# Kernel optimization log

Hardware: AMD Instinct MI355X
Metric: run time of the kernel (lower is better)

The kernel has to match this reference:

```python
import jax, jax.numpy as jnp
import numpy as np

H = 4                 # num_heads
GATE_NORM = 16.0      # gate_logit_normalizer
EPS = 1e-5            # RMSNorm eps


def setup_inputs() -> dict:
    key = jax.random.key(0)
    ks = jax.random.split(key, 12)
    B, T, D = 8, 4096, 1024
    Dk_total, Dv_total, Dlow = D // 2, D, 16

    def w(k, shape, fan_in):
        return jax.random.normal(k, shape, dtype=jnp.float32) * (fan_in ** -0.5)

    return {
        "x": jax.random.normal(ks[0], (B, T, D), dtype=jnp.float32),
        "Wq": w(ks[1], (D, Dk_total), D),
        "Wk": w(ks[2], (D, Dk_total), D),
        "Wv": w(ks[3], (D, Dv_total), D),
        "gk_w1": w(ks[4], (D, Dlow), D),
        "gk_w2": w(ks[5], (Dlow, Dk_total), Dlow),
        "gk_b2": jnp.zeros((Dk_total,), dtype=jnp.float32),
        "Wg": w(ks[6], (D, Dv_total), D),
        "g_norm_w": jnp.ones((Dv_total // H,), dtype=jnp.float32),
        "Wo": w(ks[7], (Dv_total, D), Dv_total),
    }


def _gla_forward(x, Wq, Wk, Wv, gk_w1, gk_w2, gk_b2, Wg, g_norm_w, Wo):
    B, T, D = x.shape
    Dk = Wq.shape[1] // H
    Dv = Wv.shape[1] // H

    q = (x @ Wq).reshape(B, T, H, Dk) * (Dk ** -0.5)
    k = (x @ Wk).reshape(B, T, H, Dk)
    v = (x @ Wv).reshape(B, T, H, Dv)
    # low-rank gate logits -> log-space decay gk (<= 0)
    gk = jax.nn.log_sigmoid((x @ gk_w1) @ gk_w2 + gk_b2) / GATE_NORM
    gk = gk.reshape(B, T, H, Dk)

    # recurrent gated linear attention:
    #   S_t = exp(gk_t)[:, None] * S_{t-1} + k_t^T v_t ;  o_t = q_t @ S_t
    def step(S, qkvg):
        qt, kt, vt, gt = qkvg          # each [B, H, Dk|Dv]
        S = jnp.exp(gt)[..., None] * S + kt[..., None] * vt[..., None, :]
        ot = jnp.einsum("bhk,bhkv->bhv", qt, S)
        return S, ot

    S0 = jnp.zeros((B, H, Dk, Dv), dtype=x.dtype)
    tm = lambda a: jnp.swapaxes(a, 0, 1)  # [B,T,...] -> [T,B,...]
    _, o = jax.lax.scan(step, S0, (tm(q), tm(k), tm(v), tm(gk)))
    o = jnp.swapaxes(o, 0, 1)            # [B, T, H, Dv]

    # output gate: RMSNorm(o) * swish(g), per head
    g = (x @ Wg).reshape(B, T, H, Dv)
    o = o * jax.lax.rsqrt(jnp.mean(o * o, axis=-1, keepdims=True) + EPS) * g_norm_w
    o = o * (g * jax.nn.sigmoid(g))
    return o.reshape(B, T, H * Dv) @ Wo


def reference(x, Wq, Wk, Wv, gk_w1, gk_w2, gk_b2, Wg, g_norm_w, Wo):
    return _gla_forward(x, Wq, Wk, Wv, gk_w1, gk_w2, gk_b2, Wg, g_norm_w, Wo)
```

## Files before the change

kernel.cpp:

```cpp
#include <hip/hip_runtime.h>
#include <hip/hip_bf16.h>
#include <cstdint>
#include <cstddef>

typedef __hip_bfloat16 bf16;
typedef __attribute__((ext_vector_type(8))) short short8;
typedef __attribute__((ext_vector_type(4))) float floatx4;

__device__ __forceinline__ void gload_lds16(const void* g, void* l) {
  __builtin_amdgcn_global_load_lds(
      (__attribute__((address_space(1))) void*)(uintptr_t)g,
      (__attribute__((address_space(3))) void*)l, 16, 0, 0);
}

__device__ __forceinline__ short f2bbits(float f) {
  bf16 h = __float2bfloat16(f);
  return __builtin_bit_cast(short, h);
}
__device__ __forceinline__ float b2f(short s) {
  return __bfloat162float(__builtin_bit_cast(bf16, s));
}

__global__ __launch_bounds__(256) void convert_x(const float* __restrict__ x,
                                                 bf16* __restrict__ xb) {
  size_t i = ((size_t)blockIdx.x * 256 + threadIdx.x) * 8;
  float4 f0 = *(const float4*)(x + i);
  float4 f1 = *(const float4*)(x + i + 4);
  short8 r;
  r[0] = f2bbits(f0.x); r[1] = f2bbits(f0.y); r[2] = f2bbits(f0.z); r[3] = f2bbits(f0.w);
  r[4] = f2bbits(f1.x); r[5] = f2bbits(f1.y); r[6] = f2bbits(f1.z); r[7] = f2bbits(f1.w);
  *(short8*)(xb + i) = r;
}

__global__ __launch_bounds__(256) void transpose_w(const float* __restrict__ src,
                                                   bf16* __restrict__ dst, int cols) {
  __shared__ float tile[32][33];
  int n0 = blockIdx.x * 32, k0 = blockIdx.y * 32;
  int tx = threadIdx.x & 31, ty = threadIdx.x >> 5;
#pragma unroll
  for (int i = 0; i < 32; i += 8) {
    int kk = k0 + ty + i, nn = n0 + tx;
    tile[ty + i][tx] = (nn < cols) ? src[(size_t)kk * cols + nn] : 0.0f;
  }
  __syncthreads();
#pragma unroll
  for (int i = 0; i < 32; i += 8) {
    int nn = n0 + ty + i, kk = k0 + tx;
    if (nn < cols) dst[(size_t)nn * 1024 + kk] = __float2bfloat16(tile[tx][ty + i]);
  }
}

#define BARR __builtin_amdgcn_s_barrier()
#define WAITV(n) asm volatile("s_waitcnt vmcnt(" #n ")" ::: "memory")

#define STA(buf, h, tau) do { \
  gload_lds16(pA + (size_t)(h) * K64 + (size_t)(tau) * 64, \
              &lds[(buf) * 16384 + (h) * 8192 + w * 512]); \
  gload_lds16(pA + K128 + (size_t)(h) * K64 + (size_t)(tau) * 64, \
              &lds[(buf) * 16384 + (h) * 8192 + 4096 + w * 512]); \
} while (0)

#define STB(buf, h, tau) do { \
  gload_lds16(pB + (size_t)(h) * K32 + (size_t)(tau) * 64, \
              &lds[32768 + (buf) * 16384 + (h) * 8192 + w * 512]); \
  gload_lds16(pB + K128 + (size_t)(h) * K32 + (size_t)(tau) * 64, \
              &lds[32768 + (buf) * 16384 + (h) * 8192 + 4096 + w * 512]); \
} while (0)

#define LDA(mh, buf) do { \
  _Pragma("unroll") \
  for (int mp = 0; mp < 4; ++mp) { \
    const short* p_ = &lds[(buf) * 16384 + (mh) * 8192 + aRow + mp * 1024]; \
    a[mp][0] = *(const short8*)(p_ + g0); \
    a[mp][1] = *(const short8*)(p_ + g1); \
  } \
} while (0)

#define LDB(nh, buf, d0, d1) do { \
  const short* p_ = &lds[(buf) * 16384 + (nh) * 8192 + bRow]; \
  d0[0] = *(const short8*)(p_ + g0); \
  d0[1] = *(const short8*)(p_ + g1); \
  d1[0] = *(const short8*)(p_ + 1024 + g0); \
  d1[1] = *(const short8*)(p_ + 1024 + g1); \
} while (0)

#define MQ(MB, NB, d0, d1) do { \
  __builtin_amdgcn_s_setprio(1); \
  _Pragma("unroll") \
  for (int mp = 0; mp < 4; ++mp) { \
    acc[(MB) + mp][(NB)] = __builtin_amdgcn_mfma_f32_16x16x32_bf16(a[mp][0], d0[0], acc[(MB) + mp][(NB)], 0, 0, 0); \
    acc[(MB) + mp][(NB)] = __builtin_amdgcn_mfma_f32_16x16x32_bf16(a[mp][1], d0[1], acc[(MB) + mp][(NB)], 0, 0, 0); \
    acc[(MB) + mp][(NB) + 1] = __builtin_amdgcn_mfma_f32_16x16x32_bf16(a[mp][0], d1[0], acc[(MB) + mp][(NB) + 1], 0, 0, 0); \
    acc[(MB) + mp][(NB) + 1] = __builtin_amdgcn_mfma_f32_16x16x32_bf16(a[mp][1], d1[1], acc[(MB) + mp][(NB) + 1], 0, 0, 0); \
  } \
  __builtin_amdgcn_s_setprio(0); \
} while (0)

__global__ __launch_bounds__(512, 2) void gemm256(
    const bf16* __restrict__ A, const bf16* __restrict__ Bt, const int K,
    const int nTN, const int mode,
    float* __restrict__ oq, float* __restrict__ okk, bf16* __restrict__ ov,
    bf16* __restrict__ ogg, float* __restrict__ oo) {
  extern __shared__ __align__(16) short lds[];
  const int tid = threadIdx.x;
  const int w = tid >> 6, lane = tid & 63;
  const int wr = w >> 2, wc = w & 3;
  const int l15 = lane & 15, lq = lane >> 4;
  const int e7 = lane & 7, l3 = lane >> 3;
  const int gAp = (lane & 7) ^ l3;

  const int cpx = (int)gridDim.x >> 3;
  const int bid = blockIdx.x;
  const int swz = (bid & 7) * cpx + (bid >> 3);
  const int mt = swz / nTN, nt = swz - mt * nTN;
  const int m0 = mt << 8, n0 = nt << 8;

  const size_t K64 = (size_t)K * 64, K128 = (size_t)K * 128, K32 = (size_t)K * 32;
  const bf16* pA = A + (size_t)(m0 + w * 8 + l3) * K + gAp * 8;
  const bf16* pB = Bt + (size_t)(n0 + (w >> 2) * 64 + (w & 3) * 8 + l3) * K + gAp * 8;

  const int g0 = ((lq ^ e7) & 7) * 8;
  const int g1 = (((lq + 4) ^ e7) & 7) * 8;
  const int aRow = (wr * 64 + l15) * 64;
  const int bRow = 32768 + (wc * 32 + l15) * 64;

  floatx4 acc[8][4] = {};
  short8 a[4][2], bb0[2], bb1[2], bb2[2], bb3[2];

  STA(0, 0, 0); STB(0, 0, 0); STB(0, 1, 0); STA(0, 1, 0);
  STA(1, 0, 1); STB(1, 1, 1);
  WAITV(4);
  BARR;

  const int nIter = K >> 7;
  for (int t = 0; t < nIter; ++t) {
    const bool nl = (t < nIter - 1);
    const int t1 = 2 * t + 1, t2 = 2 * t + 2, t3 = 2 * t + 3;
    LDA(0, 0); LDB(0, 0, bb0, bb1);
    STA(1, 1, t1);
    BARR; MQ(0, 0, bb0, bb1); BARR;
    LDB(1, 0, bb2, bb3);
    STB(1, 0, t1);
    BARR; MQ(0, 2, bb2, bb3); BARR;
    LDA(1, 0);
    if (nl) STA(0, 0, t2);
    BARR; MQ(4, 2, bb2, bb3); BARR;
    LDB(0, 0, bb0, bb1);
    if (nl) STB(0, 1, t2);
    BARR; MQ(4, 0, bb0, bb1);
    if (nl) { WAITV(4); } else { WAITV(0); }
    BARR;
    LDA(0, 1); LDB(0, 1, bb0, bb1);
    if (nl) STA(0, 1, t2);
    BARR; MQ(0, 0, bb0, bb1); BARR;
    LDB(1, 1, bb2, bb3);
    if (nl) STB(0, 0, t2);
    BARR; MQ(0, 2, bb2, bb3); BARR;
    LDA(1, 1);
    if (nl) STA(1, 0, t3);
    BARR; MQ(4, 2, bb2, bb3); BARR;
    LDB(0, 1, bb0, bb1);
    if (nl) STB(1, 1, t3);
    BARR; MQ(4, 0, bb0, bb1);
    if (nl) { WAITV(4); }
    BARR;
  }

  const int rq = lq * 4;
#pragma unroll
  for (int m = 0; m < 8; ++m) {
#pragma unroll
    for (int n = 0; n < 4; ++n) {
      const int col = n0 + wc * 64 + n * 16 + l15;
#pragma unroll
      for (int r = 0; r < 4; ++r) {
        const size_t row = (size_t)(m0 + wr * 128 + m * 16 + rq + r);
        const float val = acc[m][n][r];
        if (mode == 1) {
          oo[row * 1024 + col] = val;
        } else if (col < 512) {
          oq[row * 512 + col] = val * 0.08838834764831845f;
        } else if (col < 1024) {
          okk[row * 512 + (col - 512)] = val;
        } else if (col < 2048) {
          ov[row * 1024 + (col - 1024)] = __float2bfloat16(val);
        } else {
          ogg[row * 1024 + (col - 2048)] = __float2bfloat16(val);
        }
      }
    }
  }
}

__global__ __launch_bounds__(256) void gate_decay2(const float* __restrict__ x,
                                                   const float* __restrict__ w1,
                                                   const float* __restrict__ w2,
                                                   const float* __restrict__ b2,
                                                   float* __restrict__ gkout) {
  __shared__ float sp[256];
  __shared__ float sz[16];
  const int m = blockIdx.x, tid = threadIdx.x;
  const int j = tid & 15, dpart = tid >> 4;
  const float* xr = x + (size_t)m * 1024 + dpart * 64;
  float acc = 0.f;
#pragma unroll 8
  for (int e = 0; e < 64; ++e) acc = fmaf(xr[e], w1[(dpart * 64 + e) * 16 + j], acc);
  sp[tid] = acc;
  __syncthreads();
  if (tid < 16) {
    float s = 0.f;
#pragma unroll
    for (int p = 0; p < 16; ++p) s += sp[p * 16 + tid];
    sz[tid] = s;
  }
  __syncthreads();
#pragma unroll
  for (int u = 0; u < 2; ++u) {
    const int n = tid + u * 256;
    float t = b2[n];
#pragma unroll
    for (int jj = 0; jj < 16; ++jj) t = fmaf(sz[jj], w2[jj * 512 + n], t);
    const float ls = fminf(t, 0.f) - log1pf(__expf(-fabsf(t)));
    gkout[(size_t)m * 512 + n] = ls * 0.0625f;
  }
}

__global__ __launch_bounds__(128) void chunk_prep(
    const float* __restrict__ q, const float* __restrict__ k,
    const float* __restrict__ gk, bf16* __restrict__ qt,
    bf16* __restrict__ kt, float* __restrict__ dtot) {
  const int cid = blockIdx.x;
  const int c = cid & 63, h = (cid >> 6) & 3, b = cid >> 8;
  const int d = threadIdx.x;
  const size_t rowbase = ((size_t)(b * 4096 + c * 64)) * 512 + h * 128 + d;
  const size_t obase = (size_t)cid * 8192 + d;
  float bsum = 0.f;
  for (int i = 0; i < 64; ++i) {
    const size_t src = rowbase + (size_t)i * 512;
    bsum += gk[src];
    qt[obase + (size_t)i * 128] = __float2bfloat16(q[src] * __expf(bsum));
    kt[obase + (size_t)i * 128] = __float2bfloat16(k[src] * __expf(-bsum));
  }
  dtot[cid * 128 + d] = __expf(bsum);
}

__global__ __launch_bounds__(256) void chunk_intra(
    const bf16* __restrict__ qt, const bf16* __restrict__ kt,
    const float* __restrict__ dtot, const bf16* __restrict__ v,
    bf16* __restrict__ oi, bf16* __restrict__ ut) {
  __shared__ __align__(16) short lA[64 * 72];
  __shared__ __align__(16) short stg[27648];
  short* sQ = stg;
  short* sK = stg + 8704;
  short* sVT = stg;
  short* sKhT = stg + 18432;
  const int cid = blockIdx.x;
  const int c = cid & 63, h = (cid >> 6) & 3, b = cid >> 8;
  const int tid = threadIdx.x, wv = tid >> 6, lane = tid & 63;
  const int l15 = lane & 15, q8 = (lane >> 4) * 8, rq = (lane >> 4) * 4;

  {
    const int row = tid >> 2, seg = (tid & 3) * 32;
    const size_t src = (size_t)cid * 8192 + row * 128 + seg;
    const short8* qs = (const short8*)(qt + src);
    const short8* ks = (const short8*)(kt + src);
    short8* qd = (short8*)&sQ[row * 136 + seg];
    short8* kd = (short8*)&sK[row * 136 + seg];
#pragma unroll
    for (int t = 0; t < 4; ++t) { qd[t] = qs[t]; kd[t] = ks[t]; }
  }
  __syncthreads();
  {
    short8 af[4];
#pragma unroll
    for (int kf = 0; kf < 4; ++kf)
      af[kf] = *(const short8*)&sQ[(wv * 16 + l15) * 136 + kf * 32 + q8];
#pragma unroll
    for (int nt = 0; nt < 4; ++nt) {
      floatx4 accA = {0.f, 0.f, 0.f, 0.f};
#pragma unroll
      for (int kf = 0; kf < 4; ++kf) {
        short8 bfr = *(const short8*)&sK[(nt * 16 + l15) * 136 + kf * 32 + q8];
        accA = __builtin_amdgcn_mfma_f32_16x16x32_bf16(af[kf], bfr, accA, 0, 0, 0);
      }
#pragma unroll
      for (int r = 0; r < 4; ++r) {
        const int i = wv * 16 + rq + r, jj = nt * 16 + l15;
        lA[i * 72 + jj] = f2bbits(jj <= i ? accA[r] : 0.f);
      }
    }
  }
  __syncthreads();
  {
#pragma unroll
    for (int e = 0; e < 8; ++e) {
      const int idx = tid + e * 256;
      const int jj = idx >> 5, n0 = (idx & 31) * 8;
      short8 vv = *(const short8*)(v + ((size_t)(b * 4096 + c * 64 + jj)) * 1024 + h * 256 + n0);
#pragma unroll
      for (int t = 0; t < 8; ++t) sVT[(n0 + t) * 72 + jj] = vv[t];
    }
#pragma unroll
    for (int e = 0; e < 4; ++e) {
      const int idx = tid + e * 256;
      const int jj = idx >> 4, d0 = (idx & 15) * 8;
      short8 kk = *(const short8*)(kt + (size_t)cid * 8192 + jj * 128 + d0);
#pragma unroll
      for (int t = 0; t < 8; ++t)
        sKhT[(d0 + t) * 72 + jj] = f2bbits(b2f(kk[t]) * dtot[cid * 128 + d0 + t]);
    }
  }
  __syncthreads();
  {
    short8 aA0 = *(const short8*)&lA[(wv * 16 + l15) * 72 + q8];
    short8 aA1 = *(const short8*)&lA[(wv * 16 + l15) * 72 + 32 + q8];
#pragma unroll
    for (int nt = 0; nt < 16; ++nt) {
      short8 b0 = *(const short8*)&sVT[(nt * 16 + l15) * 72 + q8];
      short8 b1 = *(const short8*)&sVT[(nt * 16 + l15) * 72 + 32 + q8];
      floatx4 acc = {0.f, 0.f, 0.f, 0.f};
      acc = __builtin_amdgcn_mfma_f32_16x16x32_bf16(aA0, b0, acc, 0, 0, 0);
      acc = __builtin_amdgcn_mfma_f32_16x16x32_bf16(aA1, b1, acc, 0, 0, 0);
#pragma unroll
      for (int r = 0; r < 4; ++r) {
        const int i = wv * 16 + rq + r;
        oi[(size_t)cid * 16384 + i * 256 + nt * 16 + l15] = __builtin_bit_cast(bf16, f2bbits(acc[r]));
      }
    }
  }
  {
    short8 aV[4][2];
#pragma unroll
    for (int mt = 0; mt < 4; ++mt) {
      aV[mt][0] = *(const short8*)&sVT[(wv * 64 + mt * 16 + l15) * 72 + q8];
      aV[mt][1] = *(const short8*)&sVT[(wv * 64 + mt * 16 + l15) * 72 + 32 + q8];
    }
#pragma unroll
    for (int nt = 0; nt < 8; ++nt) {
      short8 b0 = *(const short8*)&sKhT[(nt * 16 + l15) * 72 + q8];
      short8 b1 = *(const short8*)&sKhT[(nt * 16 + l15) * 72 + 32 + q8];
#pragma unroll
      for (int mt = 0; mt < 4; ++mt) {
        floatx4 acc = {0.f, 0.f, 0.f, 0.f};
        acc = __builtin_amdgcn_mfma_f32_16x16x32_bf16(aV[mt][0], b0, acc, 0, 0, 0);
        acc = __builtin_amdgcn_mfma_f32_16x16x32_bf16(aV[mt][1], b1, acc, 0, 0, 0);
#pragma unroll
        for (int r = 0; r < 4; ++r) {
          const int vr = wv * 64 + mt * 16 + rq + r;
          ut[(size_t)cid * 32768 + vr * 128 + nt * 16 + l15] = __builtin_bit_cast(bf16, f2bbits(acc[r]));
        }
      }
    }
  }
}

__global__ __launch_bounds__(256) void state_prop(
    bf16* __restrict__ su,
    const float* __restrict__ dtot) {
  const int ng = blockIdx.x, h = blockIdx.y, b = blockIdx.z;
  const int tid = threadIdx.x;
  const int nrow = ng * 32 + (tid >> 3), kseg = (tid & 7) * 16;
  const int cid0 = (b * 4 + h) * 64;
  const size_t off = (size_t)nrow * 128 + kseg;
  size_t a = (size_t)cid0 * 32768 + off;
  float S[16];
#pragma unroll
  for (int e = 0; e < 16; ++e) S[e] = 0.f;
  short8 u0 = *(const short8*)(su + a);
  short8 u1 = *(const short8*)(su + a + 8);
  for (int c = 0; c < 64; ++c) {
    short8 un0, un1;
    if (c < 63) {
      un0 = *(const short8*)(su + a + 32768);
      un1 = *(const short8*)(su + a + 32768 + 8);
    }
    const float4 d0 = *(const float4*)(dtot + (cid0 + c) * 128 + kseg);
    const float4 d1 = *(const float4*)(dtot + (cid0 + c) * 128 + kseg + 4);
    const float4 d2 = *(const float4*)(dtot + (cid0 + c) * 128 + kseg + 8);
    const float4 d3 = *(const float4*)(dtot + (cid0 + c) * 128 + kseg + 12);
    short8 s0, s1;
#pragma unroll
    for (int e = 0; e < 8; ++e) { s0[e] = f2bbits(S[e]); s1[e] = f2bbits(S[8 + e]); }
    *(short8*)(su + a) = s0;
    *(short8*)(su + a + 8) = s1;
    const float dd[16] = {d0.x, d0.y, d0.z, d0.w, d1.x, d1.y, d1.z, d1.w,
                          d2.x, d2.y, d2.z, d2.w, d3.x, d3.y, d3.z, d3.w};
#pragma unroll
    for (int e = 0; e < 8; ++e) S[e] = fmaf(dd[e], S[e], b2f(u0[e]));
#pragma unroll
    for (int e = 0; e < 8; ++e) S[8 + e] = fmaf(dd[8 + e], S[8 + e], b2f(u1[e]));
    u0 = un0; u1 = un1;
    a += 32768;
  }
}

__global__ __launch_bounds__(256, 2) void o_inter(
    const bf16* __restrict__ qt, const bf16* __restrict__ scb,
    const bf16* __restrict__ oi, bf16* __restrict__ opre) {
  __shared__ __align__(16) short sQ[64 * 136];
  const int cid = blockIdx.x;
  const int c = cid & 63, h = (cid >> 6) & 3, b = cid >> 8;
  const int tid = threadIdx.x, wv = tid >> 6, lane = tid & 63;
  const int l15 = lane & 15, q8 = (lane >> 4) * 8, rq = (lane >> 4) * 4;
  {
    const int row = tid >> 2, seg = (tid & 3) * 32;
    const short8* qs = (const short8*)(qt + (size_t)cid * 8192 + row * 128 + seg);
    short8* qd = (short8*)&sQ[row * 136 + seg];
#pragma unroll
    for (int t = 0; t < 4; ++t) qd[t] = qs[t];
  }
  __syncthreads();
  short8 af[4][4];
#pragma unroll
  for (int i = 0; i < 4; ++i)
#pragma unroll
    for (int kf = 0; kf < 4; ++kf)
      af[i][kf] = *(const short8*)&sQ[(i * 16 + l15) * 136 + kf * 32 + q8];
  floatx4 acc[4][4] = {};
#pragma unroll
  for (int j = 0; j < 4; ++j) {
#pragma unroll
    for (int kf = 0; kf < 4; ++kf) {
      short8 bfr = *(const short8*)(scb + (size_t)cid * 32768 +
                                    (size_t)(wv * 64 + j * 16 + l15) * 128 + kf * 32 + q8);
#pragma unroll
      for (int i = 0; i < 4; ++i)
        acc[i][j] = __builtin_amdgcn_mfma_f32_16x16x32_bf16(af[i][kf], bfr, acc[i][j], 0, 0, 0);
    }
  }
  const size_t rowg0 = (size_t)(b * 4096 + c * 64);
#pragma unroll
  for (int i = 0; i < 4; ++i) {
#pragma unroll
    for (int j = 0; j < 4; ++j) {
      const int col = wv * 64 + j * 16 + l15;
#pragma unroll
      for (int r = 0; r < 4; ++r) {
        const int row = i * 16 + rq + r;
        const float val = acc[i][j][r] +
            __bfloat162float(oi[(size_t)cid * 16384 + row * 256 + col]);
        opre[(rowg0 + row) * 1024 + h * 256 + col] = __float2bfloat16(val);
      }
    }
  }
}

__global__ __launch_bounds__(1024) void norm_gate(
    const bf16* __restrict__ o, const bf16* __restrict__ g,
    const float* __restrict__ gnw, bf16* __restrict__ og) {
  __shared__ float sp[16];
  const int tid = threadIdx.x;
  const size_t idx = (size_t)blockIdx.x * 1024 + tid;
  const float f = __bfloat162float(o[idx]);
  float ss = f * f;
#pragma unroll
  for (int mm = 1; mm <= 32; mm <<= 1) ss += __shfl_xor(ss, mm);
  if ((tid & 63) == 0) sp[tid >> 6] = ss;
  __syncthreads();
  const int h4 = (tid >> 8) * 4;
  const float ms = (sp[h4] + sp[h4 + 1] + sp[h4 + 2] + sp[h4 + 3]) * (1.0f / 256.0f);
  const float scale = rsqrtf(ms + 1e-5f) * gnw[tid & 255];
  const float gv = __bfloat162float(g[idx]);
  const float sw = gv * (1.0f / (1.0f + __expf(-gv)));
  og[idx] = __float2bfloat16(f * scale * sw);
}

extern "C" void kernel_launch(void* const* d_in, const int* in_sizes, int n_in,
                              void* d_out, int out_size, void* d_ws, size_t ws_size,
                              hipStream_t stream) {
  const float* x   = (const float*)d_in[0];
  const float* Wq  = (const float*)d_in[1];
  const float* Wk  = (const float*)d_in[2];
  const float* Wv  = (const float*)d_in[3];
  const float* gw1 = (const float*)d_in[4];
  const float* gw2 = (const float*)d_in[5];
  const float* gb2 = (const float*)d_in[6];
  const float* Wg  = (const float*)d_in[7];
  const float* gnw = (const float*)d_in[8];
  const float* Wo  = (const float*)d_in[9];
  float* out = (float*)d_out;

  static bool attr_set = false;
  if (!attr_set) {
    hipFuncSetAttribute(reinterpret_cast<const void*>(gemm256),
                        hipFuncAttributeMaxDynamicSharedMemorySize, 131072);
    attr_set = true;
  }

  const size_t Mi = 1048576;
  uint8_t* w = (uint8_t*)d_ws;
  bf16*  wallT = (bf16*)(w);
  bf16*  woT   = (bf16*)(w + 6 * Mi);
  float* dtot  = (float*)(w + 8 * Mi);
  bf16*  xb    = (bf16*)(w + 9 * Mi);
  bf16*  qt    = (bf16*)(w + 9 * Mi);
  bf16*  ktb   = (bf16*)(w + 41 * Mi);
  bf16*  ogat  = (bf16*)(w + 9 * Mi);
  float* qb    = (float*)(w + 73 * Mi);
  float* kb    = (float*)(w + 137 * Mi);
  bf16*  utb   = (bf16*)(w + 73 * Mi);
  float* gkb   = (float*)(w + 201 * Mi);
  bf16*  oib   = (bf16*)(w + 201 * Mi);
  bf16*  vb    = (bf16*)(w + 265 * Mi);
  bf16*  opre  = (bf16*)(w + 265 * Mi);
  bf16*  gb    = (bf16*)(w + 329 * Mi);

  convert_x<<<dim3(16384), 256, 0, stream>>>(x, xb);
  transpose_w<<<dim3(16, 32), 256, 0, stream>>>(Wq, wallT, 512);
  transpose_w<<<dim3(16, 32), 256, 0, stream>>>(Wk, wallT + (size_t)512 * 1024, 512);
  transpose_w<<<dim3(32, 32), 256, 0, stream>>>(Wv, wallT + (size_t)1024 * 1024, 1024);
  transpose_w<<<dim3(32, 32), 256, 0, stream>>>(Wg, wallT + (size_t)2048 * 1024, 1024);
  transpose_w<<<dim3(32, 32), 256, 0, stream>>>(Wo, woT, 1024);
  gemm256<<<dim3(1536), 512, 131072, stream>>>(xb, wallT, 1024, 12, 0, qb, kb, vb, gb, nullptr);
  gate_decay2<<<dim3(32768), 256, 0, stream>>>(x, gw1, gw2, gb2, gkb);
  chunk_prep<<<dim3(2048), 128, 0, stream>>>(qb, kb, gkb, qt, ktb, dtot);
  chunk_intra<<<dim3(2048), 256, 0, stream>>>(qt, ktb, dtot, vb, oib, utb);
  state_prop<<<dim3(8, 4, 8), 256, 0, stream>>>(utb, dtot);
  o_inter<<<dim3(2048), 256, 0, stream>>>(qt, utb, oib, opre);
  norm_gate<<<dim3(32768), 1024, 0, stream>>>(opre, gb, gnw, ogat);
  gemm256<<<dim3(512), 512, 131072, stream>>>(ogat, woT, 1024, 4, 1, nullptr, nullptr, nullptr, nullptr, out);
}
```

Before: 1.190 ms.

## Specialize GEMM K, hoist LDS loads, batch gate rows, widen state-prop grid

Makes K a compile-time constant in the GEMM so address arithmetic folds. It also moves LDS operand loads earlier in the pipeline so they overlap with MFMA work. The gate-decay kernel now processes four rows per block and keeps the w1/w2 weights in registers instead of reloading them for every row. state_prop uses twice as many blocks, each thread carrying 8 state elements instead of 16, which adds parallelism for this latency-bound serial scan. Hoisting the loads raises register pressure in the GEMM, and the GEMM now only works for K=1024.

Result: faster. 1.097 ms (-7.9%).

```diff
diff --git a/kernel.cpp b/kernel.cpp
--- a/kernel.cpp
+++ b/kernel.cpp
@@ -53,17 +53,22 @@
 #define BARR __builtin_amdgcn_s_barrier()
 #define WAITV(n) asm volatile("s_waitcnt vmcnt(" #n ")" ::: "memory")
 
+#define KC 1024
+#define K64c (KC * 64)
+#define K128c (KC * 128)
+#define K32c (KC * 32)
+
 #define STA(buf, h, tau) do { \
-  gload_lds16(pA + (size_t)(h) * K64 + (size_t)(tau) * 64, \
+  gload_lds16(pA + (size_t)((h) * K64c + (tau) * 64), \
               &lds[(buf) * 16384 + (h) * 8192 + w * 512]); \
-  gload_lds16(pA + K128 + (size_t)(h) * K64 + (size_t)(tau) * 64, \
+  gload_lds16(pA + (size_t)(K128c + (h) * K64c + (tau) * 64), \
               &lds[(buf) * 16384 + (h) * 8192 + 4096 + w * 512]); \
 } while (0)
 
 #define STB(buf, h, tau) do { \
-  gload_lds16(pB + (size_t)(h) * K32 + (size_t)(tau) * 64, \
+  gload_lds16(pB + (size_t)((h) * K32c + (tau) * 64), \
               &lds[32768 + (buf) * 16384 + (h) * 8192 + w * 512]); \
-  gload_lds16(pB + K128 + (size_t)(h) * K32 + (size_t)(tau) * 64, \
+  gload_lds16(pB + (size_t)(K128c + (h) * K32c + (tau) * 64), \
               &lds[32768 + (buf) * 16384 + (h) * 8192 + 4096 + w * 512]); \
 } while (0)
 
@@ -97,7 +102,7 @@
 } while (0)
 
 __global__ __launch_bounds__(512, 2) void gemm256(
-    const bf16* __restrict__ A, const bf16* __restrict__ Bt, const int K,
+    const bf16* __restrict__ A, const bf16* __restrict__ Bt,
     const int nTN, const int mode,
     float* __restrict__ oq, float* __restrict__ okk, bf16* __restrict__ ov,
     bf16* __restrict__ ogg, float* __restrict__ oo) {
@@ -115,9 +120,8 @@
   const int mt = swz / nTN, nt = swz - mt * nTN;
   const int m0 = mt << 8, n0 = nt << 8;
 
-  const size_t K64 = (size_t)K * 64, K128 = (size_t)K * 128, K32 = (size_t)K * 32;
-  const bf16* pA = A + (size_t)(m0 + w * 8 + l3) * K + gAp * 8;
-  const bf16* pB = Bt + (size_t)(n0 + (w >> 2) * 64 + (w & 3) * 8 + l3) * K + gAp * 8;
+  const bf16* pA = A + (size_t)(m0 + w * 8 + l3) * KC + gAp * 8;
+  const bf16* pB = Bt + (size_t)(n0 + (w >> 2) * 64 + (w & 3) * 8 + l3) * KC + gAp * 8;
 
   const int g0 = ((lq ^ e7) & 7) * 8;
   const int g1 = (((lq + 4) ^ e7) & 7) * 8;
@@ -132,34 +136,28 @@
   WAITV(4);
   BARR;
 
-  const int nIter = K >> 7;
+  const int nIter = KC >> 7;
   for (int t = 0; t < nIter; ++t) {
     const bool nl = (t < nIter - 1);
     const int t1 = 2 * t + 1, t2 = 2 * t + 2, t3 = 2 * t + 3;
-    LDA(0, 0); LDB(0, 0, bb0, bb1);
+    LDA(0, 0); LDB(0, 0, bb0, bb1); LDB(1, 0, bb2, bb3);
     STA(1, 1, t1);
     BARR; MQ(0, 0, bb0, bb1); BARR;
-    LDB(1, 0, bb2, bb3);
     STB(1, 0, t1);
-    BARR; MQ(0, 2, bb2, bb3); BARR;
-    LDA(1, 0);
+    BARR; MQ(0, 2, bb2, bb3); LDA(1, 0); BARR;
     if (nl) STA(0, 0, t2);
     BARR; MQ(4, 2, bb2, bb3); BARR;
-    LDB(0, 0, bb0, bb1);
     if (nl) STB(0, 1, t2);
     BARR; MQ(4, 0, bb0, bb1);
     if (nl) { WAITV(4); } else { WAITV(0); }
     BARR;
-    LDA(0, 1); LDB(0, 1, bb0, bb1);
+    LDA(0, 1); LDB(0, 1, bb0, bb1); LDB(1, 1, bb2, bb3);
     if (nl) STA(0, 1, t2);
     BARR; MQ(0, 0, bb0, bb1); BARR;
-    LDB(1, 1, bb2, bb3);
     if (nl) STB(0, 0, t2);
-    BARR; MQ(0, 2, bb2, bb3); BARR;
-    LDA(1, 1);
+    BARR; MQ(0, 2, bb2, bb3); LDA(1, 1); BARR;
     if (nl) STA(1, 0, t3);
     BARR; MQ(4, 2, bb2, bb3); BARR;
-    LDB(0, 1, bb0, bb1);
     if (nl) STB(1, 1, t3);
     BARR; MQ(4, 0, bb0, bb1);
     if (nl) { WAITV(4); }
@@ -199,29 +197,44 @@
                                                    float* __restrict__ gkout) {
   __shared__ float sp[256];
   __shared__ float sz[16];
-  const int m = blockIdx.x, tid = threadIdx.x;
+  const int m0 = blockIdx.x * 4, tid = threadIdx.x;
   const int j = tid & 15, dpart = tid >> 4;
-  const float* xr = x + (size_t)m * 1024 + dpart * 64;
-  float acc = 0.f;
-#pragma unroll 8
-  for (int e = 0; e < 64; ++e) acc = fmaf(xr[e], w1[(dpart * 64 + e) * 16 + j], acc);
-  sp[tid] = acc;
-  __syncthreads();
-  if (tid < 16) {
-    float s = 0.f;
-#pragma unroll
-    for (int p = 0; p < 16; ++p) s += sp[p * 16 + tid];
-    sz[tid] = s;
-  }
-  __syncthreads();
-#pragma unroll
-  for (int u = 0; u < 2; ++u) {
-    const int n = tid + u * 256;
-    float t = b2[n];
-#pragma unroll
-    for (int jj = 0; jj < 16; ++jj) t = fmaf(sz[jj], w2[jj * 512 + n], t);
+  float w1r[64];
+#pragma unroll
+  for (int e = 0; e < 64; ++e) w1r[e] = w1[(dpart * 64 + e) * 16 + j];
+  float w2r[32];
+#pragma unroll
+  for (int jj = 0; jj < 16; ++jj) {
+    w2r[jj] = w2[jj * 512 + tid];
+    w2r[16 + jj] = w2[jj * 512 + tid + 256];
+  }
+  const float b2a = b2[tid], b2b = b2[tid + 256];
+  for (int r = 0; r < 4; ++r) {
+    const int m = m0 + r;
+    const float* xr = x + (size_t)m * 1024 + dpart * 64;
+    float acc = 0.f;
+#pragma unroll
+    for (int e = 0; e < 64; ++e) acc = fmaf(xr[e], w1r[e], acc);
+    sp[tid] = acc;
+    __syncthreads();
+    if (tid < 16) {
+      float s = 0.f;
+#pragma unroll
+      for (int p = 0; p < 16; ++p) s += sp[p * 16 + tid];
+      sz[tid] = s;
+    }
+    __syncthreads();
+    float t = b2a;
+#pragma unroll
+    for (int jj = 0; jj < 16; ++jj) t = fmaf(sz[jj], w2r[jj], t);
     const float ls = fminf(t, 0.f) - log1pf(__expf(-fabsf(t)));
-    gkout[(size_t)m * 512 + n] = ls * 0.0625f;
+    gkout[(size_t)m * 512 + tid] = ls * 0.0625f;
+    float t2 = b2b;
+#pragma unroll
+    for (int jj = 0; jj < 16; ++jj) t2 = fmaf(sz[jj], w2r[16 + jj], t2);
+    const float ls2 = fminf(t2, 0.f) - log1pf(__expf(-fabsf(t2)));
+    gkout[(size_t)m * 512 + tid + 256] = ls2 * 0.0625f;
+    if (r < 3) __syncthreads();
   }
 }
 
@@ -359,37 +372,26 @@
     const float* __restrict__ dtot) {
   const int ng = blockIdx.x, h = blockIdx.y, b = blockIdx.z;
   const int tid = threadIdx.x;
-  const int nrow = ng * 32 + (tid >> 3), kseg = (tid & 7) * 16;
+  const int nrow = ng * 16 + (tid >> 4), kseg = (tid & 15) * 8;
   const int cid0 = (b * 4 + h) * 64;
-  const size_t off = (size_t)nrow * 128 + kseg;
-  size_t a = (size_t)cid0 * 32768 + off;
-  float S[16];
-#pragma unroll
-  for (int e = 0; e < 16; ++e) S[e] = 0.f;
+  size_t a = (size_t)cid0 * 32768 + (size_t)nrow * 128 + kseg;
+  float S[8];
+#pragma unroll
+  for (int e = 0; e < 8; ++e) S[e] = 0.f;
   short8 u0 = *(const short8*)(su + a);
-  short8 u1 = *(const short8*)(su + a + 8);
   for (int c = 0; c < 64; ++c) {
-    short8 un0, un1;
-    if (c < 63) {
-      un0 = *(const short8*)(su + a + 32768);
-      un1 = *(const short8*)(su + a + 32768 + 8);
-    }
+    short8 un0;
+    if (c < 63) un0 = *(const short8*)(su + a + 32768);
     const float4 d0 = *(const float4*)(dtot + (cid0 + c) * 128 + kseg);
     const float4 d1 = *(const float4*)(dtot + (cid0 + c) * 128 + kseg + 4);
-    const float4 d2 = *(const float4*)(dtot + (cid0 + c) * 128 + kseg + 8);
-    const float4 d3 = *(const float4*)(dtot + (cid0 + c) * 128 + kseg + 12);
-    short8 s0, s1;
-#pragma unroll
-    for (int e = 0; e < 8; ++e) { s0[e] = f2bbits(S[e]); s1[e] = f2bbits(S[8 + e]); }
+    short8 s0;
+#pragma unroll
+    for (int e = 0; e < 8; ++e) s0[e] = f2bbits(S[e]);
     *(short8*)(su + a) = s0;
-    *(short8*)(su + a + 8) = s1;
-    const float dd[16] = {d0.x, d0.y, d0.z, d0.w, d1.x, d1.y, d1.z, d1.w,
-                          d2.x, d2.y, d2.z, d2.w, d3.x, d3.y, d3.z, d3.w};
+    const float dd[8] = {d0.x, d0.y, d0.z, d0.w, d1.x, d1.y, d1.z, d1.w};
 #pragma unroll
     for (int e = 0; e < 8; ++e) S[e] = fmaf(dd[e], S[e], b2f(u0[e]));
-#pragma unroll
-    for (int e = 0; e < 8; ++e) S[8 + e] = fmaf(dd[8 + e], S[8 + e], b2f(u1[e]));
-    u0 = un0; u1 = un1;
+    u0 = un0;
     a += 32768;
   }
 }
@@ -511,12 +513,12 @@
   transpose_w<<<dim3(32, 32), 256, 0, stream>>>(Wv, wallT + (size_t)1024 * 1024, 1024);
   transpose_w<<<dim3(32, 32), 256, 0, stream>>>(Wg, wallT + (size_t)2048 * 1024, 1024);
   transpose_w<<<dim3(32, 32), 256, 0, stream>>>(Wo, woT, 1024);
-  gemm256<<<dim3(1536), 512, 131072, stream>>>(xb, wallT, 1024, 12, 0, qb, kb, vb, gb, nullptr);
-  gate_decay2<<<dim3(32768), 256, 0, stream>>>(x, gw1, gw2, gb2, gkb);
+  gemm256<<<dim3(1536), 512, 131072, stream>>>(xb, wallT, 12, 0, qb, kb, vb, gb, nullptr);
+  gate_decay2<<<dim3(8192), 256, 0, stream>>>(x, gw1, gw2, gb2, gkb);
   chunk_prep<<<dim3(2048), 128, 0, stream>>>(qb, kb, gkb, qt, ktb, dtot);
   chunk_intra<<<dim3(2048), 256, 0, stream>>>(qt, ktb, dtot, vb, oib, utb);
-  state_prop<<<dim3(8, 4, 8), 256, 0, stream>>>(utb, dtot);
+  state_prop<<<dim3(16, 4, 8), 256, 0, stream>>>(utb, dtot);
   o_inter<<<dim3(2048), 256, 0, stream>>>(qt, utb, oib, opre);
   norm_gate<<<dim3(32768), 1024, 0, stream>>>(opre, gb, gnw, ogat);
-  gemm256<<<dim3(512), 512, 131072, stream>>>(ogat, woT, 1024, 4, 1, nullptr, nullptr, nullptr, nullptr, out);
-}
+  gemm256<<<dim3(512), 512, 131072, stream>>>(ogat, woT, 4, 1, nullptr, nullptr, nullptr, nullptr, out);
+}
```
